# Optimization experiments

Measured on AMD Instinct MI355X. Metric: run time of the kernel, lower is better.

Reference implementation:

```python
import jax, jax.numpy as jnp
import numpy as np

N_NODES = 50000
N_EDGES = 800000
NUM_FEATURES = 128
DIM_HIDDEN = 128
DIM_OUT = 64


def setup_inputs() -> dict:
    key = jax.random.key(0)
    k = jax.random.split(key, 5)
    x = jax.random.normal(k[0], (N_NODES, NUM_FEATURES), dtype=jnp.float32)
    edge_index = jax.random.randint(k[1], (2, N_EDGES), 0, N_NODES, dtype=jnp.int32)
    W1 = jax.random.normal(k[2], (NUM_FEATURES, DIM_HIDDEN), dtype=jnp.float32) * (1.0 / np.sqrt(NUM_FEATURES))
    b1 = jnp.zeros((DIM_HIDDEN,), dtype=jnp.float32)
    W2 = jax.random.normal(k[3], (DIM_HIDDEN, DIM_OUT), dtype=jnp.float32) * (1.0 / np.sqrt(DIM_HIDDEN))
    b2 = jnp.zeros((DIM_OUT,), dtype=jnp.float32)
    return {"x": x, "edge_index": edge_index, "W1": W1, "b1": b1, "W2": W2, "b2": b2}


def _gcn_conv(x, W, b, src, dst, n_nodes):
    # PyG GCNConv: out = D^{-1/2} (A+I) D^{-1/2} X W + b (self-loops already in src/dst)
    deg = jax.ops.segment_sum(jnp.ones_like(dst, dtype=x.dtype), dst, num_segments=n_nodes)
    dinv = jax.lax.rsqrt(jnp.maximum(deg, 1.0))  # deg >= 1 thanks to self-loops
    norm = dinv[src] * dinv[dst]                 # [E]
    xw = x @ W                                   # dense GEMM on nodes [N, out]
    msg = xw[src] * norm[:, None]                # gather + edge-wise scale [E, out]
    out = jax.ops.segment_sum(msg, dst, num_segments=n_nodes)  # scatter-add
    return out + b


def reference(x, edge_index, W1, b1, W2, b2):
    n = x.shape[0]
    loops = jnp.arange(n, dtype=edge_index.dtype)
    src = jnp.concatenate([edge_index[0], loops])
    dst = jnp.concatenate([edge_index[1], loops])
    h = _gcn_conv(x, W1, b1, src, dst, n)
    h = jax.nn.relu(h)
    h = _gcn_conv(h, W2, b2, src, dst, n)
    return jax.nn.log_softmax(h, axis=1)
```

## Files before the change

### kernel.cpp

```cpp
#include <hip/hip_runtime.h>
#include <cstdint>
#include <cstddef>


#define N_FEAT 128
#define NWAVE 8192

typedef short bf16x8 __attribute__((ext_vector_type(8)));
typedef float f32x4 __attribute__((ext_vector_type(4)));

__device__ __forceinline__ unsigned f2bf(float f) {
  unsigned u = __float_as_uint(f);
  return (u + 0x7FFFu + ((u >> 16) & 1u)) >> 16;
}
__device__ __forceinline__ float bflo(unsigned u) { return __uint_as_float(u << 16); }
__device__ __forceinline__ float bfhi(unsigned u) { return __uint_as_float(u & 0xFFFF0000u); }


__global__ void k_hist(const int* __restrict__ dst, int* __restrict__ cnt,
                       int* __restrict__ rank, int E) {
  int e = blockIdx.x * blockDim.x + threadIdx.x;
  if (e < E) rank[e] = atomicAdd(&cnt[dst[e]], 1);
}

__global__ __launch_bounds__(256) void k_bsum(const int* __restrict__ cnt,
                                              int* __restrict__ bsum, int n) {
  int i = blockIdx.x * 256 + threadIdx.x;
  int v = (i < n) ? ((cnt[i] + 3) & ~3) : 0;
  for (int o = 32; o > 0; o >>= 1) v += __shfl_down(v, o);
  __shared__ int w[4];
  if ((threadIdx.x & 63) == 0) w[threadIdx.x >> 6] = v;
  __syncthreads();
  if (threadIdx.x == 0) bsum[blockIdx.x] = w[0] + w[1] + w[2] + w[3];
}

__global__ __launch_bounds__(256) void k_bscan(const int* __restrict__ bsum,
                                               int* __restrict__ bbase, int nb) {
  __shared__ int lds[256];
  int t = threadIdx.x;
  int v = (t < nb) ? bsum[t] : 0;
  lds[t] = v;
  __syncthreads();
  for (int o = 1; o < 256; o <<= 1) {
    int u = (t >= o) ? lds[t - o] : 0;
    __syncthreads();
    lds[t] += u;
    __syncthreads();
  }
  if (t < nb) bbase[t] = lds[t] - v;
}

__global__ __launch_bounds__(256) void k_scan2(const int* __restrict__ cnt,
                                               const int* __restrict__ bbase,
                                               int* __restrict__ rowptr,
                                               float* __restrict__ dinv,
                                               unsigned* __restrict__ desc, int n) {
  __shared__ int lds[256];
  int t = threadIdx.x;
  int i = blockIdx.x * 256 + t;
  int c  = (i < n) ? cnt[i] : 0;
  int pc = (c + 3) & ~3;
  lds[t] = pc;
  __syncthreads();
  for (int o = 1; o < 256; o <<= 1) {
    int u = (t >= o) ? lds[t - o] : 0;
    __syncthreads();
    lds[t] += u;
    __syncthreads();
  }
  if (i < n) {
    int excl = bbase[blockIdx.x] + lds[t] - pc;
    rowptr[i] = excl;
    dinv[i] = rsqrtf((float)(c + 1));
    for (int p = excl + c; p < excl + pc; ++p) desc[p] = 0;
    if (i == n - 1) rowptr[n] = excl + pc;
  }
}

__global__ void k_wstart(const int* __restrict__ rowptr, int* __restrict__ wstart, int n) {
  int w = blockIdx.x * blockDim.x + threadIdx.x;
  if (w > NWAVE) return;
  if (w == NWAVE) { wstart[w] = n; return; }
  long long target = (long long)rowptr[n] * w / NWAVE;
  int lo = 0, hi = n;
  while (lo < hi) {
    int mid = (lo + hi) >> 1;
    if (rowptr[mid] < (int)target) lo = mid + 1; else hi = mid;
  }
  wstart[w] = lo;
}

__global__ void k_fill(const int* __restrict__ src, const int* __restrict__ dst,
                       const int* __restrict__ rank, const int* __restrict__ rowptr,
                       const float* __restrict__ dinv,
                       unsigned* __restrict__ desc, int E) {
  int e = blockIdx.x * blockDim.x + threadIdx.x;
  if (e >= E) return;
  int s = src[e], d = dst[e];
  int p = rowptr[d] + rank[e];
  desc[p] = (f2bf(dinv[s] * dinv[d]) << 16) | (unsigned)s;
}

template<int NCOL, bool XF32>
__global__ __launch_bounds__(256) void k_gemm_mfma(const void* __restrict__ Xv,
                                                   const float* __restrict__ W,
                                                   unsigned short* __restrict__ Yb,
                                                   int n) {
  constexpr int NT = NCOL / 16;
  __shared__ uint4 Xl[64][16];
  __shared__ uint4 Wl[NCOL][16];
  int t = threadIdx.x;
  int row0 = blockIdx.x * 64;

  for (int c = t; c < 1024; c += 256) {
    int lr = c >> 4, kc = c & 15;
    int row = row0 + lr;
    uint4 v = {0u, 0u, 0u, 0u};
    if (row < n) {
      if constexpr (XF32) {
        const float* Xf = (const float*)Xv;
        float4 f0 = *(const float4*)(Xf + (size_t)row * 128 + kc * 8);
        float4 f1 = *(const float4*)(Xf + (size_t)row * 128 + kc * 8 + 4);
        v.x = f2bf(f0.x) | (f2bf(f0.y) << 16);
        v.y = f2bf(f0.z) | (f2bf(f0.w) << 16);
        v.z = f2bf(f1.x) | (f2bf(f1.y) << 16);
        v.w = f2bf(f1.z) | (f2bf(f1.w) << 16);
      } else {
        v = ((const uint4*)Xv)[(size_t)row * 16 + kc];
      }
    }
    Xl[lr][kc ^ (lr & 7)] = v;
  }
  {
    int j = t % NCOL, kc0 = t / NCOL;
    for (int kc = kc0; kc < 16; kc += 256 / NCOL) {
      const float* wp = W + (size_t)(kc * 8) * NCOL + j;
      float f[8];
#pragma unroll
      for (int e = 0; e < 8; ++e) f[e] = wp[e * NCOL];
      uint4 v;
      v.x = f2bf(f[0]) | (f2bf(f[1]) << 16);
      v.y = f2bf(f[2]) | (f2bf(f[3]) << 16);
      v.z = f2bf(f[4]) | (f2bf(f[5]) << 16);
      v.w = f2bf(f[6]) | (f2bf(f[7]) << 16);
      Wl[j][kc ^ (j & 7)] = v;
    }
  }
  __syncthreads();

  int w = t >> 6, lane = t & 63;
  int lr16 = lane & 15, kg = lane >> 4;
  bf16x8 a[4];
#pragma unroll
  for (int kk = 0; kk < 4; ++kk)
    a[kk] = __builtin_bit_cast(bf16x8, Xl[w * 16 + lr16][(kk * 4 + kg) ^ (lane & 7)]);
#pragma unroll
  for (int jt = 0; jt < NT; ++jt) {
    f32x4 acc = {0.0f, 0.0f, 0.0f, 0.0f};
#pragma unroll
    for (int kk = 0; kk < 4; ++kk) {
      bf16x8 b = __builtin_bit_cast(bf16x8, Wl[jt * 16 + lr16][(kk * 4 + kg) ^ (lane & 7)]);
      acc = __builtin_amdgcn_mfma_f32_16x16x32_bf16(a[kk], b, acc, 0, 0, 0);
    }
    int col = jt * 16 + lr16;
#pragma unroll
    for (int r = 0; r < 4; ++r) {
      int row = row0 + w * 16 + kg * 4 + r;
      if (row < n) Yb[(size_t)row * NCOL + col] = (unsigned short)f2bf(acc[r]);
    }
  }
}


__global__ __launch_bounds__(256) void k_agg128(const unsigned* __restrict__ desc,
                                                const int* __restrict__ rowptr,
                                                const int* __restrict__ wstart,
                                                const float* __restrict__ dinv,
                                                const float* __restrict__ bias,
                                                const unsigned* __restrict__ xwb,
                                                unsigned* __restrict__ hb, int n) {
  int w    = (blockIdx.x * blockDim.x + threadIdx.x) >> 6;
  int lane = threadIdx.x & 63;
  if (w >= NWAVE) return;
  int r0 = wstart[w], r1 = wstart[w + 1];
  if (r0 >= r1) return;
  float bx0 = bias[2 * lane], bx1 = bias[2 * lane + 1];
  int beg = rowptr[r0];
  for (int r = r0; r < r1; ++r) {
    int end = rowptr[r + 1];
    float di = dinv[r];
    float sl = di * di;
    unsigned us = xwb[(size_t)r * 64 + lane];
    float ax = bx0 + bflo(us) * sl;
    float ay = bx1 + bfhi(us) * sl;
    float bx = 0.0f, by = 0.0f;
    for (int base = beg; base < end; base += 4) {
      uint4 d4 = *(const uint4*)(desc + base);
      unsigned u0 = xwb[(size_t)(d4.x & 0xFFFFu) * 64 + lane];
      unsigned u1 = xwb[(size_t)(d4.y & 0xFFFFu) * 64 + lane];
      unsigned u2 = xwb[(size_t)(d4.z & 0xFFFFu) * 64 + lane];
      unsigned u3 = xwb[(size_t)(d4.w & 0xFFFFu) * 64 + lane];
      float n0 = bfhi(d4.x), n1 = bfhi(d4.y), n2 = bfhi(d4.z), n3 = bfhi(d4.w);
      ax += bflo(u0) * n0; ay += bfhi(u0) * n0;
      bx += bflo(u1) * n1; by += bfhi(u1) * n1;
      ax += bflo(u2) * n2; ay += bfhi(u2) * n2;
      bx += bflo(u3) * n3; by += bfhi(u3) * n3;
    }
    float ox = fmaxf(ax + bx, 0.0f), oy = fmaxf(ay + by, 0.0f);
    hb[(size_t)r * 64 + lane] = f2bf(ox) | (f2bf(oy) << 16);
    beg = end;
  }
}

__global__ __launch_bounds__(256) void k_agg64ls(const unsigned* __restrict__ desc,
                                                 const int* __restrict__ rowptr,
                                                 const int* __restrict__ wstart,
                                                 const float* __restrict__ dinv,
                                                 const float* __restrict__ bias,
                                                 const unsigned* __restrict__ hwb,
                                                 float* __restrict__ out, int n) {
  int w    = (blockIdx.x * blockDim.x + threadIdx.x) >> 6;
  int lane = threadIdx.x & 63;
  if (w >= NWAVE) return;
  int r0 = wstart[w], r1 = wstart[w + 1];
  if (r0 >= r1) return;
  int c    = lane & 31;
  int half = lane >> 5;
  float bc0 = bias[2 * c], bc1 = bias[2 * c + 1];
  int beg = rowptr[r0];
  for (int r = r0; r < r1; ++r) {
    int end = rowptr[r + 1];
    float ax = 0.0f, ay = 0.0f, bx = 0.0f, by = 0.0f;
    if (half == 0) {
      float di = dinv[r];
      unsigned us = hwb[(size_t)r * 32 + c];
      ax = bc0 + bflo(us) * di * di;
      ay = bc1 + bfhi(us) * di * di;
    }
    for (int base = beg; base < end; base += 4) {
      uint4 d4 = *(const uint4*)(desc + base);
      unsigned dA = half ? d4.z : d4.x;
      unsigned dB = half ? d4.w : d4.y;
      unsigned uA = hwb[(size_t)(dA & 0xFFFFu) * 32 + c];
      unsigned uB = hwb[(size_t)(dB & 0xFFFFu) * 32 + c];
      float nA = bfhi(dA), nB = bfhi(dB);
      ax += bflo(uA) * nA; ay += bfhi(uA) * nA;
      bx += bflo(uB) * nB; by += bfhi(uB) * nB;
    }
    float vx = ax + bx, vy = ay + by;
    vx += __shfl_xor(vx, 32);
    vy += __shfl_xor(vy, 32);
    float m = fmaxf(vx, vy);
    for (int o = 16; o > 0; o >>= 1) m = fmaxf(m, __shfl_xor(m, o));
    float s = expf(vx - m) + expf(vy - m);
    for (int o = 16; o > 0; o >>= 1) s += __shfl_xor(s, o);
    float ls = logf(s);
    if (half == 0) {
      float2 o2 = { vx - m - ls, vy - m - ls };
      *(float2*)(out + (size_t)r * 64 + 2 * c) = o2;
    }
    beg = end;
  }
}

extern "C" void kernel_launch(void* const* d_in, const int* in_sizes, int n_in,
                              void* d_out, int out_size, void* d_ws, size_t ws_size,
                              hipStream_t stream) {
  const float* x  = (const float*)d_in[0];
  const int*   ei = (const int*)d_in[1];
  const float* W1 = (const float*)d_in[2];
  const float* b1 = (const float*)d_in[3];
  const float* W2 = (const float*)d_in[4];
  const float* b2 = (const float*)d_in[5];
  float* out = (float*)d_out;

  const int n = in_sizes[0] / N_FEAT;
  const int E = in_sizes[1] / 2;
  const int* src = ei;
  const int* dst = ei + E;
  const int nb = (n + 255) / 256;

  auto align = [](size_t v) { return (v + 255) & ~(size_t)255; };
  char* ws = (char*)d_ws;
  size_t off = 0;
  int*      cnt    = (int*)     (ws + off); off += align((size_t)n * 4);
  int*      rowptr = (int*)     (ws + off); off += align((size_t)(n + 1) * 4);
  float*    dinv   = (float*)   (ws + off); off += align((size_t)n * 4);
  int*      rank   = (int*)     (ws + off); off += align((size_t)E * 4);
  int*      bsum   = (int*)     (ws + off); off += align(256 * 4);
  int*      bbase  = (int*)     (ws + off); off += align(256 * 4);
  int*      wstart = (int*)     (ws + off); off += align((size_t)(NWAVE + 1) * 4);
  unsigned* desc   = (unsigned*)(ws + off); off += align((size_t)(E + 4 * n) * 4);
  unsigned* xwb    = (unsigned*)(ws + off); off += align((size_t)n * 64 * 4);
  unsigned* hb     = (unsigned*)(ws + off); off += align((size_t)n * 64 * 4);
  unsigned* hwb    = xwb;

  hipMemsetAsync(cnt, 0, (size_t)n * 4, stream);
  k_hist<<<(E + 255) / 256, 256, 0, stream>>>(dst, cnt, rank, E);
  k_bsum<<<nb, 256, 0, stream>>>(cnt, bsum, n);
  k_bscan<<<1, 256, 0, stream>>>(bsum, bbase, nb);
  k_scan2<<<nb, 256, 0, stream>>>(cnt, bbase, rowptr, dinv, desc, n);
  k_wstart<<<(NWAVE + 256) / 256, 256, 0, stream>>>(rowptr, wstart, n);
  k_fill<<<(E + 255) / 256, 256, 0, stream>>>(src, dst, rank, rowptr, dinv, desc, E);

  k_gemm_mfma<128, true><<<(n + 63) / 64, 256, 0, stream>>>(
      x, W1, (unsigned short*)xwb, n);
  k_agg128<<<NWAVE / 4, 256, 0, stream>>>(desc, rowptr, wstart, dinv, b1, xwb, hb, n);

  k_gemm_mfma<64, false><<<(n + 63) / 64, 256, 0, stream>>>(
      hb, W2, (unsigned short*)hwb, n);
  k_agg64ls<<<NWAVE / 4, 256, 0, stream>>>(desc, rowptr, wstart, dinv, b2, hwb, out, n);
}
```

Before: 231.2 us.

## Split aggregation lanes across edges and column slices with separate wave partitions

The first aggregation now assigns each wave a 16-column slice of the 128-wide features and has four lane groups process different edges in parallel, with row ranges from a coarser 2048-wave partition, four blocks per partition. The second aggregation uses four edge groups of 16 lanes each covering all 64 outputs, reduced with cross-lane shuffles before log_softmax. The aim is more independent gathers in flight per wave and better edge-level parallelism. In exchange it adds shuffle reductions, narrower 64-byte gathers per edge, and each desc entry is read by several blocks.

```diff
diff --git a/kernel.cpp b/kernel.cpp
--- a/kernel.cpp
+++ b/kernel.cpp
@@ -4,7 +4,8 @@
 
 
 #define N_FEAT 128
-#define NWAVE 8192
+#define NWAVE_A 2048
+#define NWAVE_B 8192
 
 typedef short bf16x8 __attribute__((ext_vector_type(8)));
 typedef float f32x4 __attribute__((ext_vector_type(4)));
@@ -77,17 +78,26 @@
   }
 }
 
-__global__ void k_wstart(const int* __restrict__ rowptr, int* __restrict__ wstart, int n) {
-  int w = blockIdx.x * blockDim.x + threadIdx.x;
-  if (w > NWAVE) return;
-  if (w == NWAVE) { wstart[w] = n; return; }
-  long long target = (long long)rowptr[n] * w / NWAVE;
+__device__ __forceinline__ int rp_lower_bound(const int* __restrict__ rowptr,
+                                              int n, int target) {
   int lo = 0, hi = n;
   while (lo < hi) {
     int mid = (lo + hi) >> 1;
-    if (rowptr[mid] < (int)target) lo = mid + 1; else hi = mid;
-  }
-  wstart[w] = lo;
+    if (rowptr[mid] < target) lo = mid + 1; else hi = mid;
+  }
+  return lo;
+}
+
+__global__ void k_wstart(const int* __restrict__ rowptr,
+                         int* __restrict__ wsA, int* __restrict__ wsB, int n) {
+  int w = blockIdx.x * blockDim.x + threadIdx.x;
+  int Ep = rowptr[n];
+  if (w <= NWAVE_B)
+    wsB[w] = (w == NWAVE_B) ? n
+           : rp_lower_bound(rowptr, n, (int)((long long)Ep * w / NWAVE_B));
+  if (w <= NWAVE_A)
+    wsA[w] = (w == NWAVE_A) ? n
+           : rp_lower_bound(rowptr, n, (int)((long long)Ep * w / NWAVE_A));
 }
 
 __global__ void k_fill(const int* __restrict__ src, const int* __restrict__ dst,
@@ -100,6 +110,7 @@
   int p = rowptr[d] + rank[e];
   desc[p] = (f2bf(dinv[s] * dinv[d]) << 16) | (unsigned)s;
 }
+
 
 template<int NCOL, bool XF32>
 __global__ __launch_bounds__(256) void k_gemm_mfma(const void* __restrict__ Xv,
@@ -172,92 +183,108 @@
 }
 
 
-__global__ __launch_bounds__(256) void k_agg128(const unsigned* __restrict__ desc,
-                                                const int* __restrict__ rowptr,
-                                                const int* __restrict__ wstart,
-                                                const float* __restrict__ dinv,
-                                                const float* __restrict__ bias,
-                                                const unsigned* __restrict__ xwb,
-                                                unsigned* __restrict__ hb, int n) {
-  int w    = (blockIdx.x * blockDim.x + threadIdx.x) >> 6;
-  int lane = threadIdx.x & 63;
-  if (w >= NWAVE) return;
-  int r0 = wstart[w], r1 = wstart[w + 1];
-  if (r0 >= r1) return;
-  float bx0 = bias[2 * lane], bx1 = bias[2 * lane + 1];
-  int beg = rowptr[r0];
-  for (int r = r0; r < r1; ++r) {
-    int end = rowptr[r + 1];
-    float di = dinv[r];
-    float sl = di * di;
-    unsigned us = xwb[(size_t)r * 64 + lane];
-    float ax = bx0 + bflo(us) * sl;
-    float ay = bx1 + bfhi(us) * sl;
-    float bx = 0.0f, by = 0.0f;
-    for (int base = beg; base < end; base += 4) {
-      uint4 d4 = *(const uint4*)(desc + base);
-      unsigned u0 = xwb[(size_t)(d4.x & 0xFFFFu) * 64 + lane];
-      unsigned u1 = xwb[(size_t)(d4.y & 0xFFFFu) * 64 + lane];
-      unsigned u2 = xwb[(size_t)(d4.z & 0xFFFFu) * 64 + lane];
-      unsigned u3 = xwb[(size_t)(d4.w & 0xFFFFu) * 64 + lane];
-      float n0 = bfhi(d4.x), n1 = bfhi(d4.y), n2 = bfhi(d4.z), n3 = bfhi(d4.w);
-      ax += bflo(u0) * n0; ay += bfhi(u0) * n0;
-      bx += bflo(u1) * n1; by += bfhi(u1) * n1;
-      ax += bflo(u2) * n2; ay += bfhi(u2) * n2;
-      bx += bflo(u3) * n3; by += bfhi(u3) * n3;
-    }
-    float ox = fmaxf(ax + bx, 0.0f), oy = fmaxf(ay + by, 0.0f);
-    hb[(size_t)r * 64 + lane] = f2bf(ox) | (f2bf(oy) << 16);
-    beg = end;
-  }
-}
-
-__global__ __launch_bounds__(256) void k_agg64ls(const unsigned* __restrict__ desc,
+__global__ __launch_bounds__(256) void k_agg128s(const unsigned* __restrict__ desc,
                                                  const int* __restrict__ rowptr,
-                                                 const int* __restrict__ wstart,
+                                                 const int* __restrict__ wsA,
                                                  const float* __restrict__ dinv,
                                                  const float* __restrict__ bias,
-                                                 const unsigned* __restrict__ hwb,
-                                                 float* __restrict__ out, int n) {
-  int w    = (blockIdx.x * blockDim.x + threadIdx.x) >> 6;
-  int lane = threadIdx.x & 63;
-  if (w >= NWAVE) return;
-  int r0 = wstart[w], r1 = wstart[w + 1];
+                                                 const unsigned* __restrict__ xwb,
+                                                 unsigned* __restrict__ hb, int n) {
+  int slice = blockIdx.x & 3;
+  int w     = (blockIdx.x >> 2) * 4 + (threadIdx.x >> 6);
+  int lane  = threadIdx.x & 63;
+  int q = lane >> 4, c = lane & 15;
+  int r0 = wsA[w], r1 = wsA[w + 1];
   if (r0 >= r1) return;
-  int c    = lane & 31;
-  int half = lane >> 5;
-  float bc0 = bias[2 * c], bc1 = bias[2 * c + 1];
+  int co = slice * 16 + c;
+  float b0 = bias[2 * co], b1 = bias[2 * co + 1];
   int beg = rowptr[r0];
   for (int r = r0; r < r1; ++r) {
     int end = rowptr[r + 1];
     float ax = 0.0f, ay = 0.0f, bx = 0.0f, by = 0.0f;
-    if (half == 0) {
+    if (q == 0) {
       float di = dinv[r];
-      unsigned us = hwb[(size_t)r * 32 + c];
-      ax = bc0 + bflo(us) * di * di;
-      ay = bc1 + bfhi(us) * di * di;
+      float sl = di * di;
+      unsigned us = xwb[(size_t)r * 64 + co];
+      ax = b0 + bflo(us) * sl;
+      ay = b1 + bfhi(us) * sl;
+    }
+    int base = beg;
+    for (; base + 8 <= end; base += 8) {
+      unsigned d0 = desc[base + q];
+      unsigned d1 = desc[base + 4 + q];
+      unsigned u0 = xwb[(size_t)(d0 & 0xFFFFu) * 64 + co];
+      unsigned u1 = xwb[(size_t)(d1 & 0xFFFFu) * 64 + co];
+      float n0 = bfhi(d0), n1 = bfhi(d1);
+      ax += bflo(u0) * n0; ay += bfhi(u0) * n0;
+      bx += bflo(u1) * n1; by += bfhi(u1) * n1;
+    }
+    if (base < end) {
+      unsigned d0 = desc[base + q];
+      unsigned u0 = xwb[(size_t)(d0 & 0xFFFFu) * 64 + co];
+      float n0 = bfhi(d0);
+      ax += bflo(u0) * n0; ay += bfhi(u0) * n0;
+    }
+    ax += bx; ay += by;
+    ax += __shfl_xor(ax, 16); ax += __shfl_xor(ax, 32);
+    ay += __shfl_xor(ay, 16); ay += __shfl_xor(ay, 32);
+    if (q == 0) {
+      float ox = fmaxf(ax, 0.0f), oy = fmaxf(ay, 0.0f);
+      hb[(size_t)r * 64 + co] = f2bf(ox) | (f2bf(oy) << 16);
+    }
+    beg = end;
+  }
+}
+
+__global__ __launch_bounds__(256) void k_agg64q(const unsigned* __restrict__ desc,
+                                                const int* __restrict__ rowptr,
+                                                const int* __restrict__ wsB,
+                                                const float* __restrict__ dinv,
+                                                const float* __restrict__ bias,
+                                                const unsigned* __restrict__ hwb,
+                                                float* __restrict__ out, int n) {
+  int w    = blockIdx.x * 4 + (threadIdx.x >> 6);
+  int lane = threadIdx.x & 63;
+  int q = lane >> 4, c = lane & 15;
+  int r0 = wsB[w], r1 = wsB[w + 1];
+  if (r0 >= r1) return;
+  float b0 = bias[2 * c], b1 = bias[2 * c + 1];
+  float b2 = bias[32 + 2 * c], b3 = bias[32 + 2 * c + 1];
+  int beg = rowptr[r0];
+  for (int r = r0; r < r1; ++r) {
+    int end = rowptr[r + 1];
+    float ax = 0.0f, ay = 0.0f, az = 0.0f, aw = 0.0f;
+    if (q == 0) {
+      float di = dinv[r];
+      float sl = di * di;
+      unsigned us0 = hwb[(size_t)r * 32 + c];
+      unsigned us1 = hwb[(size_t)r * 32 + 16 + c];
+      ax = b0 + bflo(us0) * sl; ay = b1 + bfhi(us0) * sl;
+      az = b2 + bflo(us1) * sl; aw = b3 + bfhi(us1) * sl;
     }
     for (int base = beg; base < end; base += 4) {
-      uint4 d4 = *(const uint4*)(desc + base);
-      unsigned dA = half ? d4.z : d4.x;
-      unsigned dB = half ? d4.w : d4.y;
-      unsigned uA = hwb[(size_t)(dA & 0xFFFFu) * 32 + c];
-      unsigned uB = hwb[(size_t)(dB & 0xFFFFu) * 32 + c];
-      float nA = bfhi(dA), nB = bfhi(dB);
-      ax += bflo(uA) * nA; ay += bfhi(uA) * nA;
-      bx += bflo(uB) * nB; by += bfhi(uB) * nB;
-    }
-    float vx = ax + bx, vy = ay + by;
-    vx += __shfl_xor(vx, 32);
-    vy += __shfl_xor(vy, 32);
-    float m = fmaxf(vx, vy);
-    for (int o = 16; o > 0; o >>= 1) m = fmaxf(m, __shfl_xor(m, o));
-    float s = expf(vx - m) + expf(vy - m);
-    for (int o = 16; o > 0; o >>= 1) s += __shfl_xor(s, o);
+      unsigned d = desc[base + q];
+      size_t sp = (size_t)(d & 0xFFFFu) * 32;
+      unsigned u0 = hwb[sp + c];
+      unsigned u1 = hwb[sp + 16 + c];
+      float nm = bfhi(d);
+      ax += bflo(u0) * nm; ay += bfhi(u0) * nm;
+      az += bflo(u1) * nm; aw += bfhi(u1) * nm;
+    }
+    ax += __shfl_xor(ax, 16); ax += __shfl_xor(ax, 32);
+    ay += __shfl_xor(ay, 16); ay += __shfl_xor(ay, 32);
+    az += __shfl_xor(az, 16); az += __shfl_xor(az, 32);
+    aw += __shfl_xor(aw, 16); aw += __shfl_xor(aw, 32);
+    float m = fmaxf(fmaxf(ax, ay), fmaxf(az, aw));
+    for (int o = 8; o > 0; o >>= 1) m = fmaxf(m, __shfl_xor(m, o));
+    float s = expf(ax - m) + expf(ay - m) + expf(az - m) + expf(aw - m);
+    for (int o = 8; o > 0; o >>= 1) s += __shfl_xor(s, o);
     float ls = logf(s);
-    if (half == 0) {
-      float2 o2 = { vx - m - ls, vy - m - ls };
-      *(float2*)(out + (size_t)r * 64 + 2 * c) = o2;
+    if (q == 0) {
+      float2 o0 = { ax - m - ls, ay - m - ls };
+      float2 o1 = { az - m - ls, aw - m - ls };
+      *(float2*)(out + (size_t)r * 64 + 2 * c) = o0;
+      *(float2*)(out + (size_t)r * 64 + 32 + 2 * c) = o1;
     }
     beg = end;
   }
@@ -289,7 +316,8 @@
   int*      rank   = (int*)     (ws + off); off += align((size_t)E * 4);
   int*      bsum   = (int*)     (ws + off); off += align(256 * 4);
   int*      bbase  = (int*)     (ws + off); off += align(256 * 4);
-  int*      wstart = (int*)     (ws + off); off += align((size_t)(NWAVE + 1) * 4);
+  int*      wsA    = (int*)     (ws + off); off += align((size_t)(NWAVE_A + 1) * 4);
+  int*      wsB    = (int*)     (ws + off); off += align((size_t)(NWAVE_B + 1) * 4);
   unsigned* desc   = (unsigned*)(ws + off); off += align((size_t)(E + 4 * n) * 4);
   unsigned* xwb    = (unsigned*)(ws + off); off += align((size_t)n * 64 * 4);
   unsigned* hb     = (unsigned*)(ws + off); off += align((size_t)n * 64 * 4);
@@ -300,14 +328,14 @@
   k_bsum<<<nb, 256, 0, stream>>>(cnt, bsum, n);
   k_bscan<<<1, 256, 0, stream>>>(bsum, bbase, nb);
   k_scan2<<<nb, 256, 0, stream>>>(cnt, bbase, rowptr, dinv, desc, n);
-  k_wstart<<<(NWAVE + 256) / 256, 256, 0, stream>>>(rowptr, wstart, n);
+  k_wstart<<<(NWAVE_B + 256) / 256, 256, 0, stream>>>(rowptr, wsA, wsB, n);
   k_fill<<<(E + 255) / 256, 256, 0, stream>>>(src, dst, rank, rowptr, dinv, desc, E);
 
   k_gemm_mfma<128, true><<<(n + 63) / 64, 256, 0, stream>>>(
       x, W1, (unsigned short*)xwb, n);
-  k_agg128<<<NWAVE / 4, 256, 0, stream>>>(desc, rowptr, wstart, dinv, b1, xwb, hb, n);
+  k_agg128s<<<NWAVE_A, 256, 0, stream>>>(desc, rowptr, wsA, dinv, b1, xwb, hb, n);
 
   k_gemm_mfma<64, false><<<(n + 63) / 64, 256, 0, stream>>>(
       hb, W2, (unsigned short*)hwb, n);
-  k_agg64ls<<<NWAVE / 4, 256, 0, stream>>>(desc, rowptr, wstart, dinv, b2, hwb, out, n);
-}
+  k_agg64q<<<NWAVE_B / 4, 256, 0, stream>>>(desc, rowptr, wsB, dinv, b2, hwb, out, n);
+}
```

New measurement: 262.1 us. +13.4%, slower.

## Bucket CSR edges by source range and aggregate bucket-major for cache locality

Applied to the files above, without the earlier changes.

Each destination's edge list is split into four sub-buckets keyed on source-index bits, so the CSR becomes per (dst, bucket). Aggregation waves now own a fixed block of 13 rows and sweep the buckets in order, keeping partial sums in LDS. While a bucket is being processed, gathers come from a narrower slice of source rows, which is meant to improve L2 reuse of the gathered feature rows. The cost is four times more row pointers and padding to multiples of four per sub-bucket, extra LDS traffic, and dropping the edge-balanced wave partitioning in favour of a fixed rows-per-wave split.

```diff
diff --git a/kernel.cpp b/kernel.cpp
--- a/kernel.cpp
+++ b/kernel.cpp
@@ -4,7 +4,7 @@
 
 
 #define N_FEAT 128
-#define NWAVE 8192
+#define RPW 13
 
 typedef short bf16x8 __attribute__((ext_vector_type(8)));
 typedef float f32x4 __attribute__((ext_vector_type(4)));
@@ -15,33 +15,43 @@
 }
 __device__ __forceinline__ float bflo(unsigned u) { return __uint_as_float(u << 16); }
 __device__ __forceinline__ float bfhi(unsigned u) { return __uint_as_float(u & 0xFFFF0000u); }
-
-
-__global__ void k_hist(const int* __restrict__ dst, int* __restrict__ cnt,
-                       int* __restrict__ rank, int E) {
+__device__ __forceinline__ int bkt(int s) { return (s >> 11) & 3; }
+
+
+__global__ void k_hist(const int* __restrict__ src, const int* __restrict__ dst,
+                       int* __restrict__ cnt2, int* __restrict__ rank, int E) {
   int e = blockIdx.x * blockDim.x + threadIdx.x;
-  if (e < E) rank[e] = atomicAdd(&cnt[dst[e]], 1);
-}
-
-__global__ __launch_bounds__(256) void k_bsum(const int* __restrict__ cnt,
-                                              int* __restrict__ bsum, int n) {
+  if (e >= E) return;
+  int key = dst[e] * 4 + bkt(src[e]);
+  rank[e] = atomicAdd(&cnt2[key], 1);
+}
+
+__global__ __launch_bounds__(256) void k_bsum(const int* __restrict__ cnt2,
+                                              int* __restrict__ bsum,
+                                              float* __restrict__ dinv,
+                                              int m, int n) {
   int i = blockIdx.x * 256 + threadIdx.x;
-  int v = (i < n) ? ((cnt[i] + 3) & ~3) : 0;
+  int v = (i < m) ? ((cnt2[i] + 3) & ~3) : 0;
   for (int o = 32; o > 0; o >>= 1) v += __shfl_down(v, o);
   __shared__ int w[4];
   if ((threadIdx.x & 63) == 0) w[threadIdx.x >> 6] = v;
   __syncthreads();
   if (threadIdx.x == 0) bsum[blockIdx.x] = w[0] + w[1] + w[2] + w[3];
-}
-
-__global__ __launch_bounds__(256) void k_bscan(const int* __restrict__ bsum,
-                                               int* __restrict__ bbase, int nb) {
-  __shared__ int lds[256];
+  int row = blockIdx.x * 64 + threadIdx.x;
+  if (threadIdx.x < 64 && row < n) {
+    int deg = cnt2[4 * row] + cnt2[4 * row + 1] + cnt2[4 * row + 2] + cnt2[4 * row + 3];
+    dinv[row] = rsqrtf((float)(deg + 1));
+  }
+}
+
+__global__ __launch_bounds__(1024) void k_bscan(const int* __restrict__ bsum,
+                                                int* __restrict__ bbase, int nb) {
+  __shared__ int lds[1024];
   int t = threadIdx.x;
   int v = (t < nb) ? bsum[t] : 0;
   lds[t] = v;
   __syncthreads();
-  for (int o = 1; o < 256; o <<= 1) {
+  for (int o = 1; o < 1024; o <<= 1) {
     int u = (t >= o) ? lds[t - o] : 0;
     __syncthreads();
     lds[t] += u;
@@ -50,15 +60,14 @@
   if (t < nb) bbase[t] = lds[t] - v;
 }
 
-__global__ __launch_bounds__(256) void k_scan2(const int* __restrict__ cnt,
+__global__ __launch_bounds__(256) void k_scan2(const int* __restrict__ cnt2,
                                                const int* __restrict__ bbase,
-                                               int* __restrict__ rowptr,
-                                               float* __restrict__ dinv,
-                                               unsigned* __restrict__ desc, int n) {
+                                               int* __restrict__ rp2,
+                                               unsigned* __restrict__ desc, int m) {
   __shared__ int lds[256];
   int t = threadIdx.x;
   int i = blockIdx.x * 256 + t;
-  int c  = (i < n) ? cnt[i] : 0;
+  int c  = (i < m) ? cnt2[i] : 0;
   int pc = (c + 3) & ~3;
   lds[t] = pc;
   __syncthreads();
@@ -68,38 +77,25 @@
     lds[t] += u;
     __syncthreads();
   }
-  if (i < n) {
+  if (i < m) {
     int excl = bbase[blockIdx.x] + lds[t] - pc;
-    rowptr[i] = excl;
-    dinv[i] = rsqrtf((float)(c + 1));
+    rp2[i] = excl;
     for (int p = excl + c; p < excl + pc; ++p) desc[p] = 0;
-    if (i == n - 1) rowptr[n] = excl + pc;
-  }
-}
-
-__global__ void k_wstart(const int* __restrict__ rowptr, int* __restrict__ wstart, int n) {
-  int w = blockIdx.x * blockDim.x + threadIdx.x;
-  if (w > NWAVE) return;
-  if (w == NWAVE) { wstart[w] = n; return; }
-  long long target = (long long)rowptr[n] * w / NWAVE;
-  int lo = 0, hi = n;
-  while (lo < hi) {
-    int mid = (lo + hi) >> 1;
-    if (rowptr[mid] < (int)target) lo = mid + 1; else hi = mid;
-  }
-  wstart[w] = lo;
+    if (i == m - 1) rp2[m] = excl + pc;
+  }
 }
 
 __global__ void k_fill(const int* __restrict__ src, const int* __restrict__ dst,
-                       const int* __restrict__ rank, const int* __restrict__ rowptr,
+                       const int* __restrict__ rank, const int* __restrict__ rp2,
                        const float* __restrict__ dinv,
                        unsigned* __restrict__ desc, int E) {
   int e = blockIdx.x * blockDim.x + threadIdx.x;
   if (e >= E) return;
   int s = src[e], d = dst[e];
-  int p = rowptr[d] + rank[e];
+  int p = rp2[d * 4 + bkt(s)] + rank[e];
   desc[p] = (f2bf(dinv[s] * dinv[d]) << 16) | (unsigned)s;
 }
+
 
 template<int NCOL, bool XF32>
 __global__ __launch_bounds__(256) void k_gemm_mfma(const void* __restrict__ Xv,
@@ -159,8 +155,8 @@
     f32x4 acc = {0.0f, 0.0f, 0.0f, 0.0f};
 #pragma unroll
     for (int kk = 0; kk < 4; ++kk) {
-      bf16x8 b = __builtin_bit_cast(bf16x8, Wl[jt * 16 + lr16][(kk * 4 + kg) ^ (lane & 7)]);
-      acc = __builtin_amdgcn_mfma_f32_16x16x32_bf16(a[kk], b, acc, 0, 0, 0);
+      bf16x8 bb = __builtin_bit_cast(bf16x8, Wl[jt * 16 + lr16][(kk * 4 + kg) ^ (lane & 7)]);
+      acc = __builtin_amdgcn_mfma_f32_16x16x32_bf16(a[kk], bb, acc, 0, 0, 0);
     }
     int col = jt * 16 + lr16;
 #pragma unroll
@@ -172,82 +168,113 @@
 }
 
 
-__global__ __launch_bounds__(256) void k_agg128(const unsigned* __restrict__ desc,
-                                                const int* __restrict__ rowptr,
-                                                const int* __restrict__ wstart,
+__global__ __launch_bounds__(256) void k_agg128L(const unsigned* __restrict__ desc,
+                                                 const int* __restrict__ rp2,
+                                                 const float* __restrict__ dinv,
+                                                 const float* __restrict__ bias,
+                                                 const unsigned* __restrict__ xwb,
+                                                 unsigned* __restrict__ hb, int n) {
+  __shared__ float2 acc2[4][RPW][64];
+  int wq   = threadIdx.x >> 6;
+  int lane = threadIdx.x & 63;
+  int wv   = blockIdx.x * 4 + wq;
+  int gr0  = wv * RPW;
+  if (gr0 >= n) return;
+  float b0 = bias[2 * lane], b1 = bias[2 * lane + 1];
+  for (int r = 0; r < RPW; ++r) {
+    int gr = gr0 + r;
+    if (gr >= n) break;
+    float di = dinv[gr];
+    float sl = di * di;
+    unsigned us = xwb[(size_t)gr * 64 + lane];
+    acc2[wq][r][lane] = make_float2(b0 + bflo(us) * sl, b1 + bfhi(us) * sl);
+  }
+  for (int b = 0; b < 4; ++b) {
+    for (int r = 0; r < RPW; ++r) {
+      int gr = gr0 + r;
+      if (gr >= n) break;
+      int beg = rp2[4 * gr + b], end = rp2[4 * gr + b + 1];
+      if (beg >= end) continue;
+      float ax = 0.0f, ay = 0.0f, bx = 0.0f, by = 0.0f;
+      for (int base = beg; base < end; base += 4) {
+        uint4 d4 = *(const uint4*)(desc + base);
+        unsigned u0 = xwb[(size_t)(d4.x & 0xFFFFu) * 64 + lane];
+        unsigned u1 = xwb[(size_t)(d4.y & 0xFFFFu) * 64 + lane];
+        unsigned u2 = xwb[(size_t)(d4.z & 0xFFFFu) * 64 + lane];
+        unsigned u3 = xwb[(size_t)(d4.w & 0xFFFFu) * 64 + lane];
+        float n0 = bfhi(d4.x), n1 = bfhi(d4.y), n2 = bfhi(d4.z), n3 = bfhi(d4.w);
+        ax += bflo(u0) * n0; ay += bfhi(u0) * n0;
+        bx += bflo(u1) * n1; by += bfhi(u1) * n1;
+        ax += bflo(u2) * n2; ay += bfhi(u2) * n2;
+        bx += bflo(u3) * n3; by += bfhi(u3) * n3;
+      }
+      float2 a = acc2[wq][r][lane];
+      a.x += ax + bx; a.y += ay + by;
+      acc2[wq][r][lane] = a;
+    }
+  }
+  for (int r = 0; r < RPW; ++r) {
+    int gr = gr0 + r;
+    if (gr >= n) break;
+    float2 a = acc2[wq][r][lane];
+    hb[(size_t)gr * 64 + lane] = f2bf(fmaxf(a.x, 0.0f)) | (f2bf(fmaxf(a.y, 0.0f)) << 16);
+  }
+}
+
+__global__ __launch_bounds__(256) void k_agg64L(const unsigned* __restrict__ desc,
+                                                const int* __restrict__ rp2,
                                                 const float* __restrict__ dinv,
                                                 const float* __restrict__ bias,
-                                                const unsigned* __restrict__ xwb,
-                                                unsigned* __restrict__ hb, int n) {
-  int w    = (blockIdx.x * blockDim.x + threadIdx.x) >> 6;
+                                                const unsigned* __restrict__ hwb,
+                                                float* __restrict__ out, int n) {
+  __shared__ float2 acc2[4][RPW][64];
+  int wq   = threadIdx.x >> 6;
   int lane = threadIdx.x & 63;
-  if (w >= NWAVE) return;
-  int r0 = wstart[w], r1 = wstart[w + 1];
-  if (r0 >= r1) return;
-  float bx0 = bias[2 * lane], bx1 = bias[2 * lane + 1];
-  int beg = rowptr[r0];
-  for (int r = r0; r < r1; ++r) {
-    int end = rowptr[r + 1];
-    float di = dinv[r];
-    float sl = di * di;
-    unsigned us = xwb[(size_t)r * 64 + lane];
-    float ax = bx0 + bflo(us) * sl;
-    float ay = bx1 + bfhi(us) * sl;
-    float bx = 0.0f, by = 0.0f;
-    for (int base = beg; base < end; base += 4) {
-      uint4 d4 = *(const uint4*)(desc + base);
-      unsigned u0 = xwb[(size_t)(d4.x & 0xFFFFu) * 64 + lane];
-      unsigned u1 = xwb[(size_t)(d4.y & 0xFFFFu) * 64 + lane];
-      unsigned u2 = xwb[(size_t)(d4.z & 0xFFFFu) * 64 + lane];
-      unsigned u3 = xwb[(size_t)(d4.w & 0xFFFFu) * 64 + lane];
-      float n0 = bfhi(d4.x), n1 = bfhi(d4.y), n2 = bfhi(d4.z), n3 = bfhi(d4.w);
-      ax += bflo(u0) * n0; ay += bfhi(u0) * n0;
-      bx += bflo(u1) * n1; by += bfhi(u1) * n1;
-      ax += bflo(u2) * n2; ay += bfhi(u2) * n2;
-      bx += bflo(u3) * n3; by += bfhi(u3) * n3;
-    }
-    float ox = fmaxf(ax + bx, 0.0f), oy = fmaxf(ay + by, 0.0f);
-    hb[(size_t)r * 64 + lane] = f2bf(ox) | (f2bf(oy) << 16);
-    beg = end;
-  }
-}
-
-__global__ __launch_bounds__(256) void k_agg64ls(const unsigned* __restrict__ desc,
-                                                 const int* __restrict__ rowptr,
-                                                 const int* __restrict__ wstart,
-                                                 const float* __restrict__ dinv,
-                                                 const float* __restrict__ bias,
-                                                 const unsigned* __restrict__ hwb,
-                                                 float* __restrict__ out, int n) {
-  int w    = (blockIdx.x * blockDim.x + threadIdx.x) >> 6;
-  int lane = threadIdx.x & 63;
-  if (w >= NWAVE) return;
-  int r0 = wstart[w], r1 = wstart[w + 1];
-  if (r0 >= r1) return;
+  int wv   = blockIdx.x * 4 + wq;
+  int gr0  = wv * RPW;
+  if (gr0 >= n) return;
   int c    = lane & 31;
   int half = lane >> 5;
   float bc0 = bias[2 * c], bc1 = bias[2 * c + 1];
-  int beg = rowptr[r0];
-  for (int r = r0; r < r1; ++r) {
-    int end = rowptr[r + 1];
-    float ax = 0.0f, ay = 0.0f, bx = 0.0f, by = 0.0f;
+  for (int r = 0; r < RPW; ++r) {
+    int gr = gr0 + r;
+    if (gr >= n) break;
+    float ax = 0.0f, ay = 0.0f;
     if (half == 0) {
-      float di = dinv[r];
-      unsigned us = hwb[(size_t)r * 32 + c];
+      float di = dinv[gr];
+      unsigned us = hwb[(size_t)gr * 32 + c];
       ax = bc0 + bflo(us) * di * di;
       ay = bc1 + bfhi(us) * di * di;
     }
-    for (int base = beg; base < end; base += 4) {
-      uint4 d4 = *(const uint4*)(desc + base);
-      unsigned dA = half ? d4.z : d4.x;
-      unsigned dB = half ? d4.w : d4.y;
-      unsigned uA = hwb[(size_t)(dA & 0xFFFFu) * 32 + c];
-      unsigned uB = hwb[(size_t)(dB & 0xFFFFu) * 32 + c];
-      float nA = bfhi(dA), nB = bfhi(dB);
-      ax += bflo(uA) * nA; ay += bfhi(uA) * nA;
-      bx += bflo(uB) * nB; by += bfhi(uB) * nB;
-    }
-    float vx = ax + bx, vy = ay + by;
+    acc2[wq][r][lane] = make_float2(ax, ay);
+  }
+  for (int b = 0; b < 4; ++b) {
+    for (int r = 0; r < RPW; ++r) {
+      int gr = gr0 + r;
+      if (gr >= n) break;
+      int beg = rp2[4 * gr + b], end = rp2[4 * gr + b + 1];
+      if (beg >= end) continue;
+      float ax = 0.0f, ay = 0.0f, bx = 0.0f, by = 0.0f;
+      for (int base = beg; base < end; base += 4) {
+        uint4 d4 = *(const uint4*)(desc + base);
+        unsigned dA = half ? d4.z : d4.x;
+        unsigned dB = half ? d4.w : d4.y;
+        unsigned uA = hwb[(size_t)(dA & 0xFFFFu) * 32 + c];
+        unsigned uB = hwb[(size_t)(dB & 0xFFFFu) * 32 + c];
+        float nA = bfhi(dA), nB = bfhi(dB);
+        ax += bflo(uA) * nA; ay += bfhi(uA) * nA;
+        bx += bflo(uB) * nB; by += bfhi(uB) * nB;
+      }
+      float2 a = acc2[wq][r][lane];
+      a.x += ax + bx; a.y += ay + by;
+      acc2[wq][r][lane] = a;
+    }
+  }
+  for (int r = 0; r < RPW; ++r) {
+    int gr = gr0 + r;
+    if (gr >= n) break;
+    float2 a = acc2[wq][r][lane];
+    float vx = a.x, vy = a.y;
     vx += __shfl_xor(vx, 32);
     vy += __shfl_xor(vy, 32);
     float m = fmaxf(vx, vy);
@@ -257,9 +284,8 @@
     float ls = logf(s);
     if (half == 0) {
       float2 o2 = { vx - m - ls, vy - m - ls };
-      *(float2*)(out + (size_t)r * 64 + 2 * c) = o2;
-    }
-    beg = end;
+      *(float2*)(out + (size_t)gr * 64 + 2 * c) = o2;
+    }
   }
 }
 
@@ -278,36 +304,37 @@
   const int E = in_sizes[1] / 2;
   const int* src = ei;
   const int* dst = ei + E;
-  const int nb = (n + 255) / 256;
+  const int m   = 4 * n;
+  const int nb2 = (m + 255) / 256;
+  const int nwv = (n + RPW - 1) / RPW;
+  const int nbA = (nwv + 3) / 4;
 
   auto align = [](size_t v) { return (v + 255) & ~(size_t)255; };
   char* ws = (char*)d_ws;
   size_t off = 0;
-  int*      cnt    = (int*)     (ws + off); off += align((size_t)n * 4);
-  int*      rowptr = (int*)     (ws + off); off += align((size_t)(n + 1) * 4);
-  float*    dinv   = (float*)   (ws + off); off += align((size_t)n * 4);
-  int*      rank   = (int*)     (ws + off); off += align((size_t)E * 4);
-  int*      bsum   = (int*)     (ws + off); off += align(256 * 4);
-  int*      bbase  = (int*)     (ws + off); off += align(256 * 4);
-  int*      wstart = (int*)     (ws + off); off += align((size_t)(NWAVE + 1) * 4);
-  unsigned* desc   = (unsigned*)(ws + off); off += align((size_t)(E + 4 * n) * 4);
-  unsigned* xwb    = (unsigned*)(ws + off); off += align((size_t)n * 64 * 4);
-  unsigned* hb     = (unsigned*)(ws + off); off += align((size_t)n * 64 * 4);
-  unsigned* hwb    = xwb;
-
-  hipMemsetAsync(cnt, 0, (size_t)n * 4, stream);
-  k_hist<<<(E + 255) / 256, 256, 0, stream>>>(dst, cnt, rank, E);
-  k_bsum<<<nb, 256, 0, stream>>>(cnt, bsum, n);
-  k_bscan<<<1, 256, 0, stream>>>(bsum, bbase, nb);
-  k_scan2<<<nb, 256, 0, stream>>>(cnt, bbase, rowptr, dinv, desc, n);
-  k_wstart<<<(NWAVE + 256) / 256, 256, 0, stream>>>(rowptr, wstart, n);
-  k_fill<<<(E + 255) / 256, 256, 0, stream>>>(src, dst, rank, rowptr, dinv, desc, E);
+  int*      cnt2 = (int*)     (ws + off); off += align((size_t)m * 4);
+  int*      rp2  = (int*)     (ws + off); off += align((size_t)(m + 1) * 4);
+  float*    dinv = (float*)   (ws + off); off += align((size_t)n * 4);
+  int*      rank = (int*)     (ws + off); off += align((size_t)E * 4);
+  int*      bsum = (int*)     (ws + off); off += align(1024 * 4);
+  int*      bbase= (int*)     (ws + off); off += align(1024 * 4);
+  unsigned* desc = (unsigned*)(ws + off); off += align((size_t)(E + 3 * m + 64) * 4);
+  unsigned* xwb  = (unsigned*)(ws + off); off += align((size_t)n * 64 * 4);
+  unsigned* hb   = (unsigned*)(ws + off); off += align((size_t)n * 64 * 4);
+  unsigned* hwb  = xwb;
+
+  hipMemsetAsync(cnt2, 0, (size_t)m * 4, stream);
+  k_hist<<<(E + 255) / 256, 256, 0, stream>>>(src, dst, cnt2, rank, E);
+  k_bsum<<<nb2, 256, 0, stream>>>(cnt2, bsum, dinv, m, n);
+  k_bscan<<<1, 1024, 0, stream>>>(bsum, bbase, nb2);
+  k_scan2<<<nb2, 256, 0, stream>>>(cnt2, bbase, rp2, desc, m);
+  k_fill<<<(E + 255) / 256, 256, 0, stream>>>(src, dst, rank, rp2, dinv, desc, E);
 
   k_gemm_mfma<128, true><<<(n + 63) / 64, 256, 0, stream>>>(
       x, W1, (unsigned short*)xwb, n);
-  k_agg128<<<NWAVE / 4, 256, 0, stream>>>(desc, rowptr, wstart, dinv, b1, xwb, hb, n);
+  k_agg128L<<<nbA, 256, 0, stream>>>(desc, rp2, dinv, b1, xwb, hb, n);
 
   k_gemm_mfma<64, false><<<(n + 63) / 64, 256, 0, stream>>>(
       hb, W2, (unsigned short*)hwb, n);
-  k_agg64ls<<<NWAVE / 4, 256, 0, stream>>>(desc, rowptr, wstart, dinv, b2, hwb, out, n);
-}
+  k_agg64L<<<nbA, 256, 0, stream>>>(desc, rp2, dinv, b2, hwb, out, n);
+}
```

Result: slower. 320.0 us (+38.4%).
